# Kernel tuning notes

Hardware: AMD Instinct MI355X
Metric: run time of the kernel (lower is better)

The kernel has to match this reference:

```python
import jax, jax.numpy as jnp
import numpy as np

NUM_HEADS = 16
EMBED_DIM = 1024
SEQ_LEN = 2048
BATCH = 2


def setup_inputs() -> dict:
    key = jax.random.key(0)
    ks = jax.random.split(key, 7)
    E = EMBED_DIM
    scale = 1.0 / np.sqrt(E)
    return {
        "query": jax.random.normal(ks[0], (SEQ_LEN, BATCH, E), jnp.float32),
        "key": jax.random.normal(ks[1], (SEQ_LEN, BATCH, E), jnp.float32),
        "value": jax.random.normal(ks[2], (SEQ_LEN, BATCH, E), jnp.float32),
        "in_proj_weight": jax.random.normal(ks[3], (3 * E, E), jnp.float32) * scale,
        "in_proj_bias": jnp.zeros((3 * E,), jnp.float32),
        "out_proj_weight": jax.random.normal(ks[4], (E, E), jnp.float32) * scale,
        "out_proj_bias": jnp.zeros((E,), jnp.float32),
    }


def reference(query, key, value, in_proj_weight, in_proj_bias, out_proj_weight, out_proj_bias):
    T, B, E = query.shape
    H = NUM_HEADS
    d = E // H
    scaling = float(d) ** -0.5
    # in-projections: rows [0:E) -> q, [E:2E) -> k, [2E:3E) -> v
    q = query @ in_proj_weight[:E].T + in_proj_bias[:E]
    k = key @ in_proj_weight[E:2 * E].T + in_proj_bias[E:2 * E]
    v = value @ in_proj_weight[2 * E:].T + in_proj_bias[2 * E:]
    q = q * scaling
    # (T, B, E) -> (B*H, T, d)
    q = q.reshape(T, B * H, d).transpose(1, 0, 2)
    k = k.reshape(T, B * H, d).transpose(1, 0, 2)
    v = v.reshape(T, B * H, d).transpose(1, 0, 2)
    S = k.shape[1]
    scores = jnp.einsum('ntd,nsd->nts', q, k)  # (B*H, T, S)
    attn = jax.nn.softmax(scores, axis=-1)
    out = jnp.einsum('nts,nsd->ntd', attn, v)  # (B*H, T, d)
    out = out.transpose(1, 0, 2).reshape(T, B, E)
    out = out @ out_proj_weight.T + out_proj_bias
    attn_avg = attn.reshape(B, H, T, S).sum(axis=1) / H
    return out, attn_avg
```

## Files before the change

### kernel.cpp

```cpp
#include <hip/hip_runtime.h>
#include <math.h>

#define T_LEN 2048
#define BATCH 2
#define EMB 1024
#define NHEAD 16
#define HDIM 64
#define BH (BATCH*NHEAD)
#define MROWS (T_LEN*BATCH)
#define QSCALE (0.125f * 1.4426950408889634f)
#define HEADBUF ((size_t)BH*T_LEN*HDIM)

typedef __attribute__((ext_vector_type(8))) short bf16x8;
typedef __attribute__((ext_vector_type(4))) float f32x4;

#define MFMA16(a,b,c) __builtin_amdgcn_mfma_f32_16x16x32_bf16(a,b,c,0,0,0)

__device__ __forceinline__ short f2bf(float f) {
    union { float f; unsigned u; } v; v.f = f;
    unsigned r = (v.u + 0x7FFFu + ((v.u >> 16) & 1u)) >> 16;
    return (short)(unsigned short)r;
}
__device__ __forceinline__ float bf2f(short s) {
    union { unsigned u; float f; } v; v.u = ((unsigned)(unsigned short)s) << 16;
    return v.f;
}
__device__ __forceinline__ unsigned cvtpk(float a, float b) {
    unsigned r;
    asm("v_cvt_pk_bf16_f32 %0, %1, %2" : "=v"(r) : "v"(a), "v"(b));
    return r;
}
__device__ __forceinline__ void gload16(const void* g, void* l) {
    __builtin_amdgcn_global_load_lds(
        (const __attribute__((address_space(1))) unsigned*)g,
        (__attribute__((address_space(3))) unsigned*)l, 16, 0, 0);
}

__global__ __launch_bounds__(256) void tobf16_kernel(
    const float* __restrict__ q, const float* __restrict__ k,
    const float* __restrict__ v, const float* __restrict__ w,
    const float* __restrict__ wo, short* __restrict__ out)
{
    size_t i8 = ((size_t)blockIdx.x * 256 + threadIdx.x) * 8;
    const float* src; size_t off;
    if (i8 < 12582912) {
        int sel = (int)(i8 >> 22);
        src = (sel == 0) ? q : (sel == 1) ? k : v;
        off = i8 & 4194303;
    } else if (i8 < 15728640) {
        src = w;  off = i8 - 12582912;
    } else {
        src = wo; off = i8 - 15728640;
    }
    float4 f0 = *(const float4*)(src + off);
    float4 f1 = *(const float4*)(src + off + 4);
    bf16x8 o;
    o[0]=f2bf(f0.x); o[1]=f2bf(f0.y); o[2]=f2bf(f0.z); o[3]=f2bf(f0.w);
    o[4]=f2bf(f1.x); o[5]=f2bf(f1.y); o[6]=f2bf(f1.z); o[7]=f2bf(f1.w);
    *(bf16x8*)(out + i8) = o;
}

__global__ __launch_bounds__(256) void inproj_gemm(
    const short* __restrict__ Xq, const short* __restrict__ Xk,
    const short* __restrict__ Xv, const short* __restrict__ Wb,
    const float* __restrict__ bias,
    short* __restrict__ qbuf, short* __restrict__ kbuf, short* __restrict__ vbufT)
{
    const int lin = blockIdx.y * 32 + blockIdx.x;
    const int tl  = (lin & 7) * 96 + (lin >> 3);
    const int mBase = (tl & 31) * 128;
    const int nBase = (tl >> 5) * 128;
    const int which = nBase >> 10;
    const short* __restrict__ X = (which == 0) ? Xq : (which == 1) ? Xk : Xv;

    __shared__ short Ast[2][128][32];
    __shared__ short Bst[2][128][32];

    const int tid  = threadIdx.x;
    const int lane = tid & 63;
    const int w    = tid >> 6;
    const int wr   = w >> 1, wc = w & 1;
    const int lr   = lane & 15, lg = lane >> 4;

    const int srow = lane >> 2;
    const int schk = (lane & 3) ^ ((lane >> 3) & 3);
    const int fchk = (lg ^ ((lr >> 1) & 3)) * 16;

    f32x4 acc[4][4] = {};

    #pragma unroll
    for (int j = 0; j < 2; ++j) {
        int r = j * 64 + w * 16 + srow;
        gload16(X  + (size_t)(mBase + r) * EMB + schk * 8,
                (char*)Ast[0] + j * 4096 + w * 1024);
        gload16(Wb + (size_t)(nBase + r) * EMB + schk * 8,
                (char*)Bst[0] + j * 4096 + w * 1024);
    }
    __syncthreads();

    int cur = 0;
    for (int kb = 0; kb < EMB; kb += 32) {
        if (kb + 32 < EMB) {
            #pragma unroll
            for (int j = 0; j < 2; ++j) {
                int r = j * 64 + w * 16 + srow;
                gload16(X  + (size_t)(mBase + r) * EMB + kb + 32 + schk * 8,
                        (char*)Ast[cur ^ 1] + j * 4096 + w * 1024);
                gload16(Wb + (size_t)(nBase + r) * EMB + kb + 32 + schk * 8,
                        (char*)Bst[cur ^ 1] + j * 4096 + w * 1024);
            }
        }
        bf16x8 af[4], bfr[4];
        #pragma unroll
        for (int rg = 0; rg < 4; ++rg)
            af[rg] = *(const bf16x8*)((char*)Ast[cur] + (wr * 64 + rg * 16 + lr) * 64 + fchk);
        #pragma unroll
        for (int cg = 0; cg < 4; ++cg)
            bfr[cg] = *(const bf16x8*)((char*)Bst[cur] + (wc * 64 + cg * 16 + lr) * 64 + fchk);
        #pragma unroll
        for (int rg = 0; rg < 4; ++rg)
            #pragma unroll
            for (int cg = 0; cg < 4; ++cg)
                acc[rg][cg] = MFMA16(af[rg], bfr[cg], acc[rg][cg]);
        __syncthreads();
        cur ^= 1;
    }

    #pragma unroll
    for (int rg = 0; rg < 4; ++rg) {
        #pragma unroll
        for (int cg = 0; cg < 4; ++cg) {
            int n  = nBase + wc * 64 + cg * 16 + lr;
            int e  = n & 1023;
            int h  = e >> 6, dd = e & 63;
            float bs = bias[n];
            #pragma unroll
            for (int ri = 0; ri < 4; ++ri) {
                int m = mBase + wr * 64 + rg * 16 + lg * 4 + ri;
                int t = m >> 1, b = m & 1;
                float val = acc[rg][cg][ri] + bs;
                short bfv;
                if (which == 0) { bfv = f2bf(val * QSCALE);
                    qbuf[((size_t)(b * NHEAD + h) * T_LEN + t) * HDIM + dd] = bfv; }
                else if (which == 1) { bfv = f2bf(val);
                    kbuf[((size_t)(b * NHEAD + h) * T_LEN + t) * HDIM + dd] = bfv; }
                else { bfv = f2bf(val);
                    vbufT[((size_t)(b * NHEAD + h) * HDIM + dd) * T_LEN + t] = bfv; }
            }
        }
    }
}

__global__ __launch_bounds__(256) void flash_kernel(
    const short* __restrict__ qb, const short* __restrict__ kbuf,
    const short* __restrict__ vbufT, short* __restrict__ h1,
    short* __restrict__ h2, float* __restrict__ mlws)
{
    const int qt = blockIdx.x;
    const int hb = blockIdx.y;

    __shared__ short Kst[64][64];
    __shared__ short Vst[64][64];
    __shared__ short Pst[64][72];

    const int tid  = threadIdx.x;
    const int lane = tid & 63;
    const int w    = tid >> 6;
    const int lr   = lane & 15, lg = lane >> 4;

    bf16x8 qa0, qa1;
    {
        const short* qsrc = qb + ((size_t)hb * T_LEN + qt * 64 + w * 16 + lr) * HDIM;
        qa0 = *(const bf16x8*)(qsrc + lg * 8);
        qa1 = *(const bf16x8*)(qsrc + 32 + lg * 8);
    }

    const short* kbase = kbuf  + (size_t)hb * T_LEN * HDIM;
    const short* vbase = vbufT + (size_t)hb * HDIM * T_LEN;

    const int krow = lane >> 3;
    const int kc16 = (lane & 7) ^ krow;
    const int rb0 = ((0 + lg) ^ (lr & 7)) * 16;
    const int rb1 = ((4 + lg) ^ (lr & 7)) * 16;

    float l_r = 0.f;
    f32x4 o_acc[4] = {};

    for (int st = 0; st < T_LEN / 64; ++st) {
        __syncthreads();
        #pragma unroll
        for (int it = 0; it < 2; ++it) {
            int r = (w * 2 + it) * 8 + krow;
            gload16(kbase + (size_t)(st * 64 + r) * HDIM + kc16 * 8,
                    (char*)Kst + (w * 2 + it) * 1024);
            gload16(vbase + (size_t)r * T_LEN + st * 64 + kc16 * 8,
                    (char*)Vst + (w * 2 + it) * 1024);
        }
        __syncthreads();

        f32x4 sc[4] = {};
        #pragma unroll
        for (int sg = 0; sg < 4; ++sg) {
            const char* krowp = (const char*)Kst + (sg * 16 + lr) * 128;
            bf16x8 kf0 = *(const bf16x8*)(krowp + rb0);
            bf16x8 kf1 = *(const bf16x8*)(krowp + rb1);
            sc[sg] = MFMA16(kf0, qa0, sc[sg]);
            sc[sg] = MFMA16(kf1, qa1, sc[sg]);
        }

        float p[4][4];
        #pragma unroll
        for (int sg = 0; sg < 4; ++sg)
            #pragma unroll
            for (int ri = 0; ri < 4; ++ri) {
                p[sg][ri] = exp2f(sc[sg][ri]);
                l_r += p[sg][ri];
            }

        #pragma unroll
        for (int sg = 0; sg < 4; ++sg) {
            uint2 pk;
            pk.x = cvtpk(p[sg][0], p[sg][1]);
            pk.y = cvtpk(p[sg][2], p[sg][3]);
            *(uint2*)&Pst[w * 16 + lr][sg * 16 + lg * 4] = pk;
        }

        #pragma unroll
        for (int ks = 0; ks < 2; ++ks) {
            bf16x8 pa = *(const bf16x8*)&Pst[w * 16 + lr][ks * 32 + lg * 8];
            #pragma unroll
            for (int dsub = 0; dsub < 4; ++dsub) {
                const char* vrowp = (const char*)Vst + (dsub * 16 + lr) * 128;
                bf16x8 vf = *(const bf16x8*)(vrowp + (ks ? rb1 : rb0));
                o_acc[dsub] = MFMA16(pa, vf, o_acc[dsub]);
            }
        }
    }

    float lsum = l_r;
    lsum += __shfl_xor(lsum, 16);
    lsum += __shfl_xor(lsum, 32);
    float inv = 1.0f / lsum;
    float invq[4];
    #pragma unroll
    for (int ri = 0; ri < 4; ++ri) invq[ri] = __shfl(inv, lg * 20 + ri);
    #pragma unroll
    for (int ri = 0; ri < 4; ++ri) {
        int row = qt * 64 + w * 16 + lg * 4 + ri;
        #pragma unroll
        for (int dsub = 0; dsub < 4; ++dsub) {
            float x = o_acc[dsub][ri] * invq[ri];
            size_t idx = ((size_t)hb * T_LEN + row) * HDIM + dsub * 16 + lr;
            short a = f2bf(x);
            h1[idx] = a;
            h2[idx] = f2bf(x - bf2f(a));
        }
    }
    if (lg == 0) {
        int row = qt * 64 + w * 16 + lr;
        mlws[(size_t)hb * T_LEN + row] = __log2f(lsum);
    }
}

__global__ __launch_bounds__(256) void avg_kernel(
    const short* __restrict__ qbuf, const short* __restrict__ kbuf,
    const float* __restrict__ mlws, float* __restrict__ attn_avg)
{
    const int st = blockIdx.x;
    const int qt = blockIdx.y;
    const int b  = blockIdx.z;

    __shared__ short K2[2][2][64][64];

    const int tid  = threadIdx.x;
    const int lane = tid & 63;
    const int w    = tid >> 6;
    const int lr   = lane & 15, lg = lane >> 4;
    const int srow = tid >> 3;
    const int scol = (tid & 7) * 8;

    f32x4 acc[4] = {};

    #pragma unroll
    for (int hh = 0; hh < 2; ++hh) {
        int hb0 = b * NHEAD + hh;
        #pragma unroll
        for (int j = 0; j < 2; ++j)
            gload16(kbuf + ((size_t)hb0 * T_LEN + st * 64 + j * 32 + srow) * HDIM + scol,
                    (char*)K2[0][hh] + j * 4096 + w * 1024);
    }
    __syncthreads();

    int cur = 0;
    for (int rnd = 0; rnd < 8; ++rnd) {
        if (rnd + 1 < 8) {
            #pragma unroll
            for (int hh = 0; hh < 2; ++hh) {
                int hbn = b * NHEAD + (rnd + 1) * 2 + hh;
                #pragma unroll
                for (int j = 0; j < 2; ++j)
                    gload16(kbuf + ((size_t)hbn * T_LEN + st * 64 + j * 32 + srow) * HDIM + scol,
                            (char*)K2[cur ^ 1][hh] + j * 4096 + w * 1024);
            }
        }
        #pragma unroll
        for (int hh = 0; hh < 2; ++hh) {
            int hb = b * NHEAD + rnd * 2 + hh;
            const short* qsrc = qbuf + ((size_t)hb * T_LEN + qt * 64 + w * 16 + lr) * HDIM;
            bf16x8 qa0 = *(const bf16x8*)(qsrc + lg * 8);
            bf16x8 qa1 = *(const bf16x8*)(qsrc + 32 + lg * 8);

            f32x4 sc[4] = {};
            #pragma unroll
            for (int sg = 0; sg < 4; ++sg) {
                bf16x8 kf0 = *(const bf16x8*)&K2[cur][hh][sg * 16 + lr][lg * 8];
                bf16x8 kf1 = *(const bf16x8*)&K2[cur][hh][sg * 16 + lr][32 + lg * 8];
                sc[sg] = MFMA16(qa0, kf0, sc[sg]);
                sc[sg] = MFMA16(qa1, kf1, sc[sg]);
            }

            #pragma unroll
            for (int ri = 0; ri < 4; ++ri) {
                int row = qt * 64 + w * 16 + lg * 4 + ri;
                float ml = mlws[(size_t)hb * T_LEN + row];
                #pragma unroll
                for (int sg = 0; sg < 4; ++sg)
                    acc[sg][ri] += exp2f(sc[sg][ri] - ml);
            }
        }
        __syncthreads();
        cur ^= 1;
    }

    const float invH = 1.0f / (float)NHEAD;
    #pragma unroll
    for (int ri = 0; ri < 4; ++ri) {
        int row = qt * 64 + w * 16 + lg * 4 + ri;
        #pragma unroll
        for (int sg = 0; sg < 4; ++sg)
            attn_avg[((size_t)b * T_LEN + row) * T_LEN + st * 64 + sg * 16 + lr] =
                acc[sg][ri] * invH;
    }
}

__global__ __launch_bounds__(256) void outproj_gemm(
    const short* __restrict__ h1, const short* __restrict__ h2,
    const short* __restrict__ Wob, const float* __restrict__ bo,
    float* __restrict__ out)
{
    const int lin = blockIdx.y * 32 + blockIdx.x;
    const int tl  = (lin & 7) * 32 + (lin >> 3);
    const int mBase = (tl & 31) * 128;
    const int nBase = (tl >> 5) * 128;

    __shared__ short A1st[128][64];
    __shared__ short A2st[128][64];
    __shared__ short Bst [128][64];

    const int tid  = threadIdx.x;
    const int lane = tid & 63;
    const int w    = tid >> 6;
    const int wr   = w >> 1, wc = w & 1;
    const int lr   = lane & 15, lg = lane >> 4;
    const int srow = tid >> 3;
    const int scol = (tid & 7) * 8;

    f32x4 acc[4][4] = {};

    for (int kb = 0; kb < EMB; kb += 64) {
        const int h = kb >> 6;
        __syncthreads();
        #pragma unroll
        for (int j = 0; j < 4; ++j) {
            int m = mBase + j * 32 + srow;
            int t = m >> 1, b = m & 1;
            size_t aoff = ((size_t)(b * NHEAD + h) * T_LEN + t) * HDIM + scol;
            gload16(h1 + aoff, (char*)A1st + j * 4096 + w * 1024);
            gload16(h2 + aoff, (char*)A2st + j * 4096 + w * 1024);
            gload16(Wob + (size_t)(nBase + j * 32 + srow) * EMB + kb + scol,
                    (char*)Bst + j * 4096 + w * 1024);
        }
        __syncthreads();
        #pragma unroll
        for (int ks = 0; ks < 2; ++ks) {
            bf16x8 a1[4], a2[4], bfr[4];
            #pragma unroll
            for (int rg = 0; rg < 4; ++rg) {
                a1[rg] = *(const bf16x8*)&A1st[wr * 64 + rg * 16 + lr][ks * 32 + lg * 8];
                a2[rg] = *(const bf16x8*)&A2st[wr * 64 + rg * 16 + lr][ks * 32 + lg * 8];
            }
            #pragma unroll
            for (int cg = 0; cg < 4; ++cg)
                bfr[cg] = *(const bf16x8*)&Bst[wc * 64 + cg * 16 + lr][ks * 32 + lg * 8];
            #pragma unroll
            for (int rg = 0; rg < 4; ++rg)
                #pragma unroll
                for (int cg = 0; cg < 4; ++cg) {
                    acc[rg][cg] = MFMA16(a1[rg], bfr[cg], acc[rg][cg]);
                    acc[rg][cg] = MFMA16(a2[rg], bfr[cg], acc[rg][cg]);
                }
        }
    }

    #pragma unroll
    for (int rg = 0; rg < 4; ++rg) {
        #pragma unroll
        for (int cg = 0; cg < 4; ++cg) {
            int n = nBase + wc * 64 + cg * 16 + lr;
            float bs = bo[n];
            #pragma unroll
            for (int ri = 0; ri < 4; ++ri) {
                int m = mBase + wr * 64 + rg * 16 + lg * 4 + ri;
                out[(size_t)m * EMB + n] = acc[rg][cg][ri] + bs;
            }
        }
    }
}

extern "C" void kernel_launch(void* const* d_in, const int* in_sizes, int n_in,
                              void* d_out, int out_size, void* d_ws, size_t ws_size,
                              hipStream_t stream)
{
    const float* query = (const float*)d_in[0];
    const float* key   = (const float*)d_in[1];
    const float* value = (const float*)d_in[2];
    const float* ipw   = (const float*)d_in[3];
    const float* ipb   = (const float*)d_in[4];
    const float* opw   = (const float*)d_in[5];
    const float* opb   = (const float*)d_in[6];

    short* qb  = (short*)d_ws;
    short* kb  = qb + HEADBUF;
    short* vbT = kb + HEADBUF;
    short* h1  = vbT + HEADBUF;
    short* h2  = h1 + HEADBUF;
    short* xvb = h2 + HEADBUF;
    short* wbf = xvb + HEADBUF;
    short* wob = wbf + (size_t)3 * EMB * EMB;
    float* mlws = (float*)(wob + (size_t)EMB * EMB);

    float* out      = (float*)d_out;
    float* attn_avg = out + (size_t)MROWS * EMB;

    tobf16_kernel<<<8192, 256, 0, stream>>>(query, key, value, ipw, opw, h1);
    inproj_gemm  <<<dim3(MROWS / 128, 3 * EMB / 128), 256, 0, stream>>>(
        h1, h2, xvb, wbf, ipb, qb, kb, vbT);
    flash_kernel <<<dim3(T_LEN / 64, BH),             256, 0, stream>>>(
        qb, kb, vbT, h1, h2, mlws);
    avg_kernel   <<<dim3(T_LEN / 64, T_LEN / 64, BATCH), 256, 0, stream>>>(
        qb, kb, mlws, attn_avg);
    outproj_gemm <<<dim3(MROWS / 128, EMB / 128),     256, 0, stream>>>(
        h1, h2, wob, opb, out);
}
```

Baseline: 226.8 us.

## Double-buffer flash K/V tiles, add MFMA priority hints, drop GEMM tile swizzle

The flash kernel now double-buffers its K and V tiles in shared memory and prefetches the next tile before computing the current one, so global loads overlap with MFMA work and one barrier per iteration is removed. The P staging buffer shrinks to half width by writing and consuming P in two k-halves. s_setprio hints are placed around the MFMA sections in the flash and attention-average kernels. The block-index swizzle in the in-projection and out-projection GEMMs is removed in favour of plain blockIdx mapping, which may hurt L2 locality.

```diff
diff --git a/kernel.cpp b/kernel.cpp
--- a/kernel.cpp
+++ b/kernel.cpp
@@ -66,10 +66,8 @@
     const float* __restrict__ bias,
     short* __restrict__ qbuf, short* __restrict__ kbuf, short* __restrict__ vbufT)
 {
-    const int lin = blockIdx.y * 32 + blockIdx.x;
-    const int tl  = (lin & 7) * 96 + (lin >> 3);
-    const int mBase = (tl & 31) * 128;
-    const int nBase = (tl >> 5) * 128;
+    const int mBase = blockIdx.x * 128;
+    const int nBase = blockIdx.y * 128;
     const int which = nBase >> 10;
     const short* __restrict__ X = (which == 0) ? Xq : (which == 1) ? Xk : Xv;
 
@@ -159,9 +157,9 @@
     const int qt = blockIdx.x;
     const int hb = blockIdx.y;
 
-    __shared__ short Kst[64][64];
-    __shared__ short Vst[64][64];
-    __shared__ short Pst[64][72];
+    __shared__ short Kst[2][64][64];
+    __shared__ short Vst[2][64][64];
+    __shared__ short Pst[64][40];
 
     const int tid  = threadIdx.x;
     const int lane = tid & 63;
@@ -186,27 +184,40 @@
     float l_r = 0.f;
     f32x4 o_acc[4] = {};
 
+    #pragma unroll
+    for (int it = 0; it < 2; ++it) {
+        int r = (w * 2 + it) * 8 + krow;
+        gload16(kbase + (size_t)r * HDIM + kc16 * 8,
+                (char*)Kst[0] + (w * 2 + it) * 1024);
+        gload16(vbase + (size_t)r * T_LEN + kc16 * 8,
+                (char*)Vst[0] + (w * 2 + it) * 1024);
+    }
+    __syncthreads();
+
+    int cur = 0;
     for (int st = 0; st < T_LEN / 64; ++st) {
-        __syncthreads();
-        #pragma unroll
-        for (int it = 0; it < 2; ++it) {
-            int r = (w * 2 + it) * 8 + krow;
-            gload16(kbase + (size_t)(st * 64 + r) * HDIM + kc16 * 8,
-                    (char*)Kst + (w * 2 + it) * 1024);
-            gload16(vbase + (size_t)r * T_LEN + st * 64 + kc16 * 8,
-                    (char*)Vst + (w * 2 + it) * 1024);
-        }
-        __syncthreads();
+        if (st + 1 < T_LEN / 64) {
+            #pragma unroll
+            for (int it = 0; it < 2; ++it) {
+                int r = (w * 2 + it) * 8 + krow;
+                gload16(kbase + (size_t)((st + 1) * 64 + r) * HDIM + kc16 * 8,
+                        (char*)Kst[cur ^ 1] + (w * 2 + it) * 1024);
+                gload16(vbase + (size_t)r * T_LEN + (st + 1) * 64 + kc16 * 8,
+                        (char*)Vst[cur ^ 1] + (w * 2 + it) * 1024);
+            }
+        }
 
         f32x4 sc[4] = {};
+        __builtin_amdgcn_s_setprio(1);
         #pragma unroll
         for (int sg = 0; sg < 4; ++sg) {
-            const char* krowp = (const char*)Kst + (sg * 16 + lr) * 128;
+            const char* krowp = (const char*)Kst[cur] + (sg * 16 + lr) * 128;
             bf16x8 kf0 = *(const bf16x8*)(krowp + rb0);
             bf16x8 kf1 = *(const bf16x8*)(krowp + rb1);
             sc[sg] = MFMA16(kf0, qa0, sc[sg]);
             sc[sg] = MFMA16(kf1, qa1, sc[sg]);
         }
+        __builtin_amdgcn_s_setprio(0);
 
         float p[4][4];
         #pragma unroll
@@ -218,23 +229,28 @@
             }
 
         #pragma unroll
-        for (int sg = 0; sg < 4; ++sg) {
-            uint2 pk;
-            pk.x = cvtpk(p[sg][0], p[sg][1]);
-            pk.y = cvtpk(p[sg][2], p[sg][3]);
-            *(uint2*)&Pst[w * 16 + lr][sg * 16 + lg * 4] = pk;
-        }
-
-        #pragma unroll
         for (int ks = 0; ks < 2; ++ks) {
-            bf16x8 pa = *(const bf16x8*)&Pst[w * 16 + lr][ks * 32 + lg * 8];
+            #pragma unroll
+            for (int sgh = 0; sgh < 2; ++sgh) {
+                int sg = ks * 2 + sgh;
+                uint2 pk;
+                pk.x = cvtpk(p[sg][0], p[sg][1]);
+                pk.y = cvtpk(p[sg][2], p[sg][3]);
+                *(uint2*)&Pst[w * 16 + lr][sgh * 16 + lg * 4] = pk;
+            }
+            bf16x8 pa = *(const bf16x8*)&Pst[w * 16 + lr][lg * 8];
+            __builtin_amdgcn_s_setprio(1);
             #pragma unroll
             for (int dsub = 0; dsub < 4; ++dsub) {
-                const char* vrowp = (const char*)Vst + (dsub * 16 + lr) * 128;
+                const char* vrowp = (const char*)Vst[cur] + (dsub * 16 + lr) * 128;
                 bf16x8 vf = *(const bf16x8*)(vrowp + (ks ? rb1 : rb0));
                 o_acc[dsub] = MFMA16(pa, vf, o_acc[dsub]);
             }
-        }
+            __builtin_amdgcn_s_setprio(0);
+        }
+
+        __syncthreads();
+        cur ^= 1;
     }
 
     float lsum = l_r;
@@ -311,6 +327,7 @@
             bf16x8 qa1 = *(const bf16x8*)(qsrc + 32 + lg * 8);
 
             f32x4 sc[4] = {};
+            __builtin_amdgcn_s_setprio(1);
             #pragma unroll
             for (int sg = 0; sg < 4; ++sg) {
                 bf16x8 kf0 = *(const bf16x8*)&K2[cur][hh][sg * 16 + lr][lg * 8];
@@ -318,6 +335,7 @@
                 sc[sg] = MFMA16(qa0, kf0, sc[sg]);
                 sc[sg] = MFMA16(qa1, kf1, sc[sg]);
             }
+            __builtin_amdgcn_s_setprio(0);
 
             #pragma unroll
             for (int ri = 0; ri < 4; ++ri) {
@@ -348,10 +366,8 @@
     const short* __restrict__ Wob, const float* __restrict__ bo,
     float* __restrict__ out)
 {
-    const int lin = blockIdx.y * 32 + blockIdx.x;
-    const int tl  = (lin & 7) * 32 + (lin >> 3);
-    const int mBase = (tl & 31) * 128;
-    const int nBase = (tl >> 5) * 128;
+    const int mBase = blockIdx.x * 128;
+    const int nBase = blockIdx.y * 128;
 
     __shared__ short A1st[128][64];
     __shared__ short A2st[128][64];
```

After: 215.6 us. 4.9% less time.

## Keep softmax probabilities in registers via permuted V layout; drop block swizzles

Applied to the files above, without the earlier changes.

The V projection now writes its transposed buffer with a within-32 permutation of the sequence index. This lets the flash kernel pack P straight from the score accumulators into MFMA A-operands and skip the LDS round-trip through a Pst buffer. The XCD-aware block remapping in both projection GEMMs is removed in favour of plain blockIdx tiling. setprio is wrapped around the score MFMAs in the attention-average kernel. Removing the remapping may reduce L2 locality across chiplets, and the permutation must match the accumulator layout exactly for results to stay correct.

```diff
diff --git a/kernel.cpp b/kernel.cpp
--- a/kernel.cpp
+++ b/kernel.cpp
@@ -66,10 +66,8 @@
     const float* __restrict__ bias,
     short* __restrict__ qbuf, short* __restrict__ kbuf, short* __restrict__ vbufT)
 {
-    const int lin = blockIdx.y * 32 + blockIdx.x;
-    const int tl  = (lin & 7) * 96 + (lin >> 3);
-    const int mBase = (tl & 31) * 128;
-    const int nBase = (tl >> 5) * 128;
+    const int mBase = blockIdx.x * 128;
+    const int nBase = blockIdx.y * 128;
     const int which = nBase >> 10;
     const short* __restrict__ X = (which == 0) ? Xq : (which == 1) ? Xk : Xv;
 
@@ -144,8 +142,13 @@
                     qbuf[((size_t)(b * NHEAD + h) * T_LEN + t) * HDIM + dd] = bfv; }
                 else if (which == 1) { bfv = f2bf(val);
                     kbuf[((size_t)(b * NHEAD + h) * T_LEN + t) * HDIM + dd] = bfv; }
-                else { bfv = f2bf(val);
-                    vbufT[((size_t)(b * NHEAD + h) * HDIM + dd) * T_LEN + t] = bfv; }
+                else {
+                    bfv = f2bf(val);
+                    int s5 = t & 31;
+                    int kk = ((s5 >> 2) & 3) * 8 + ((s5 >> 4) << 2) + (s5 & 3);
+                    int tt = (t & ~31) | kk;
+                    vbufT[((size_t)(b * NHEAD + h) * HDIM + dd) * T_LEN + tt] = bfv;
+                }
             }
         }
     }
@@ -161,7 +164,6 @@
 
     __shared__ short Kst[64][64];
     __shared__ short Vst[64][64];
-    __shared__ short Pst[64][72];
 
     const int tid  = threadIdx.x;
     const int lane = tid & 63;
@@ -218,21 +220,17 @@
             }
 
         #pragma unroll
-        for (int sg = 0; sg < 4; ++sg) {
-            uint2 pk;
-            pk.x = cvtpk(p[sg][0], p[sg][1]);
-            pk.y = cvtpk(p[sg][2], p[sg][3]);
-            *(uint2*)&Pst[w * 16 + lr][sg * 16 + lg * 4] = pk;
-        }
-
-        #pragma unroll
         for (int ks = 0; ks < 2; ++ks) {
-            bf16x8 pa = *(const bf16x8*)&Pst[w * 16 + lr][ks * 32 + lg * 8];
+            union { unsigned u[4]; bf16x8 v; } pau;
+            pau.u[0] = cvtpk(p[ks * 2][0],     p[ks * 2][1]);
+            pau.u[1] = cvtpk(p[ks * 2][2],     p[ks * 2][3]);
+            pau.u[2] = cvtpk(p[ks * 2 + 1][0], p[ks * 2 + 1][1]);
+            pau.u[3] = cvtpk(p[ks * 2 + 1][2], p[ks * 2 + 1][3]);
             #pragma unroll
             for (int dsub = 0; dsub < 4; ++dsub) {
                 const char* vrowp = (const char*)Vst + (dsub * 16 + lr) * 128;
                 bf16x8 vf = *(const bf16x8*)(vrowp + (ks ? rb1 : rb0));
-                o_acc[dsub] = MFMA16(pa, vf, o_acc[dsub]);
+                o_acc[dsub] = MFMA16(pau.v, vf, o_acc[dsub]);
             }
         }
     }
@@ -311,6 +309,7 @@
             bf16x8 qa1 = *(const bf16x8*)(qsrc + 32 + lg * 8);
 
             f32x4 sc[4] = {};
+            __builtin_amdgcn_s_setprio(1);
             #pragma unroll
             for (int sg = 0; sg < 4; ++sg) {
                 bf16x8 kf0 = *(const bf16x8*)&K2[cur][hh][sg * 16 + lr][lg * 8];
@@ -318,6 +317,7 @@
                 sc[sg] = MFMA16(qa0, kf0, sc[sg]);
                 sc[sg] = MFMA16(qa1, kf1, sc[sg]);
             }
+            __builtin_amdgcn_s_setprio(0);
 
             #pragma unroll
             for (int ri = 0; ri < 4; ++ri) {
@@ -348,10 +348,8 @@
     const short* __restrict__ Wob, const float* __restrict__ bo,
     float* __restrict__ out)
 {
-    const int lin = blockIdx.y * 32 + blockIdx.x;
-    const int tl  = (lin & 7) * 32 + (lin >> 3);
-    const int mBase = (tl & 31) * 128;
-    const int nBase = (tl >> 5) * 128;
+    const int mBase = blockIdx.x * 128;
+    const int nBase = blockIdx.y * 128;
 
     __shared__ short A1st[128][64];
     __shared__ short A2st[128][64];
```

Result: faster. 208.5 us (-8.1%).
